# Optimization experiments

Hardware: AMD Instinct MI355X
Metric: run time of the kernel (lower is better)

The kernel has to match this reference:

```python
import jax, jax.numpy as jnp
import numpy as np

N_NODES = 50000
N_EDGES = 800000
DIM_FEAT = 96
INFO_DIM = 32
DIM_EMB = 160
CONV_OUT = DIM_EMB - INFO_DIM  # 128
NUM_LAYERS = 3
NUM_GRAPHS = 500
DIM_TARGET = 10


def setup_inputs() -> dict:
    key = jax.random.key(0)
    ks = jax.random.split(key, 20)
    inp = {
        'x': jax.random.normal(ks[0], (N_NODES, DIM_FEAT), dtype=jnp.float32),
        'edge_index': jax.random.randint(ks[1], (2, N_EDGES), 0, N_NODES, dtype=jnp.int32),
        'batch': jnp.sort(jax.random.randint(ks[2], (N_NODES,), 0, NUM_GRAPHS, dtype=jnp.int32)),
        'struc_info': jax.random.normal(ks[3], (NUM_GRAPHS, INFO_DIM), dtype=jnp.float32),
    }
    # SAGEConv params per layer: lin_l (on aggregated neighbors, with bias), lin_r (on root, no bias)
    in_dims = [DIM_FEAT + INFO_DIM, DIM_EMB, DIM_EMB]
    k = 4
    for i, din in enumerate(in_dims):
        s = 1.0 / np.sqrt(din)
        inp[f'Wl{i}'] = jax.random.uniform(ks[k], (din, CONV_OUT), jnp.float32, -s, s); k += 1
        inp[f'Wr{i}'] = jax.random.uniform(ks[k], (din, CONV_OUT), jnp.float32, -s, s); k += 1
        inp[f'b{i}'] = jax.random.uniform(ks[k], (CONV_OUT,), jnp.float32, -s, s); k += 1
    s1 = 1.0 / np.sqrt(NUM_LAYERS * CONV_OUT)
    inp['Wfc1'] = jax.random.uniform(ks[k], (NUM_LAYERS * CONV_OUT, DIM_EMB), jnp.float32, -s1, s1); k += 1
    inp['bfc1'] = jax.random.uniform(ks[k], (DIM_EMB,), jnp.float32, -s1, s1); k += 1
    s2 = 1.0 / np.sqrt(DIM_EMB)
    inp['Wfc2'] = jax.random.uniform(ks[k], (DIM_EMB, DIM_TARGET), jnp.float32, -s2, s2); k += 1
    inp['bfc2'] = jax.random.uniform(ks[k], (DIM_TARGET,), jnp.float32, -s2, s2)
    return inp


def _sage_conv(h, src, dst, Wl, Wr, b, n_nodes):
    # PyG SAGEConv (mean aggr): out = lin_l(mean_{j in N(i)} x_j) + lin_r(x_i)
    agg = jax.ops.segment_sum(h[src], dst, num_segments=n_nodes)       # [N, D]
    deg = jax.ops.segment_sum(jnp.ones_like(dst, dtype=h.dtype), dst, num_segments=n_nodes)
    mean = agg / jnp.maximum(deg, 1.0)[:, None]
    return mean @ Wl + b + h @ Wr


def reference(x, edge_index, batch, struc_info, Wl0, Wr0, b0, Wl1, Wr1, b1, Wl2, Wr2, b2, Wfc1, bfc1, Wfc2, bfc2):
    n_nodes = x.shape[0]
    src, dst = edge_index[0], edge_index[1]
    info = struc_info[batch]                         # [N, info_dim] repeated per node
    params = [(Wl0, Wr0, b0), (Wl1, Wr1, b1), (Wl2, Wr2, b2)]
    h = x
    outs = []
    for (Wl, Wr, b) in params:
        h = _sage_conv(jnp.concatenate([h, info], axis=1), src, dst, Wl, Wr, b, n_nodes)
        outs.append(h)
    hcat = jnp.concatenate(outs, axis=1)             # [N, num_layers*conv_out]
    g = jax.ops.segment_max(hcat, batch, num_segments=struc_info.shape[0])  # global max pool
    z = jax.nn.relu(g @ Wfc1 + bfc1)
    return z @ Wfc2 + bfc2
```

## Files before the change

### kernel.cpp

```cpp
#include <hip/hip_runtime.h>
#include <hip/hip_bf16.h>
#include <float.h>

#define NN 50000
#define NE 800000
#define DF 96
#define DI 32
#define CO 128
#define NG 500
#define F1I 384
#define F1O 160
#define F2O 10
#define CAPLOG 7
#define NRANGE 196
#define EPB 3125
#define RCAPLOG 13
#define GGEMM 391

typedef unsigned int  u32;
typedef unsigned short u16;
typedef short bf16x8 __attribute__((ext_vector_type(8)));
typedef float f32x4  __attribute__((ext_vector_type(4)));

__device__ __forceinline__ u16 f2b(float f) {
    __hip_bfloat16 h = __float2bfloat16(f);
    return *reinterpret_cast<u16*>(&h);
}
__device__ __forceinline__ float blo(u32 u) { return __uint_as_float(u << 16); }
__device__ __forceinline__ float bhi(u32 u) { return __uint_as_float(u & 0xffff0000u); }

struct P {
    const float* x; const int* batch; const float* info;
    const int* src; const int* dst;
    const float *Wl0, *Wr0, *b0, *Wl1, *Wr1, *b1, *Wl2, *Wr2, *b2;
    const float *Wfc1, *bfc1, *Wfc2, *bfc2;
    float* out;
    int* grescnt; u32* ebin; int* start; u16* xb;
    u16 *WT0, *WT1, *WT2;
    float *iQl0, *iQr0, *iQl1, *iQr1, *iQl2, *iQr2;
    int* cnt; u16* csr;
    u16 *h1, *h2, *h3, *zlp, *zq;
    float* gpart;
};


__device__ void sec_binA(int vb, const int* __restrict__ src, const int* __restrict__ dst,
                         int* __restrict__ grescnt, u32* __restrict__ ebin, char* smem) {
    u32* pairs = (u32*)smem;
    int* lcnt  = (int*)(smem + EPB * 4);
    int t = threadIdx.x;
    int base = vb * EPB;
    lcnt[t] = 0;
    __syncthreads();
    for (int j = t; j < EPB; j += 256) {
        int e = base + j;
        int d = dst[e];
        int s = src[e];
        pairs[j] = ((u32)(d & 255) << 24) | ((u32)(d >> 8) << 16) | (u32)s;
        atomicAdd(&lcnt[d >> 8], 1);
    }
    __syncthreads();
    int myCnt = lcnt[t];
    int myBase = atomicAdd(&grescnt[t * 16], myCnt);
    __syncthreads();
    lcnt[t] = myBase;
    __syncthreads();
    for (int j = t; j < EPB; j += 256) {
        u32 pr = pairs[j];
        int r = (pr >> 16) & 255;
        int pos = atomicAdd(&lcnt[r], 1);
        if (pos < (1 << RCAPLOG)) ebin[(r << RCAPLOG) + pos] = pr;
    }
}

__device__ void sec_starts(int vb, const int* __restrict__ batch, int* __restrict__ start) {
    int i = vb * 256 + threadIdx.x;
    if (i >= NN) return;
    int b = batch[i];
    if (i == 0) { for (int g = 0; g <= b; ++g) start[g] = 0; }
    else {
        int p = batch[i - 1];
        if (p != b) for (int g = p + 1; g <= b; ++g) start[g] = i;
    }
    if (i == NN - 1) { for (int g = b + 1; g <= NG; ++g) start[g] = NN; }
}

__device__ void sec_binB(int r, const u32* __restrict__ ebin, const int* __restrict__ grescnt,
                         int* __restrict__ cnt, u16* __restrict__ csr, char* smem) {
    int* lcnt = (int*)smem;
    int t = threadIdx.x;
    lcnt[t] = 0;
    __syncthreads();
    int total = grescnt[r * 16];
    if (total > (1 << RCAPLOG)) total = 1 << RCAPLOG;
    for (int j = t; j < total; j += 256) {
        u32 p = ebin[(r << RCAPLOG) + j];
        int dloc = p >> 24;
        int rank = atomicAdd(&lcnt[dloc], 1);
        int node = (r << 8) + dloc;
        if (rank < (1 << CAPLOG)) csr[(node << CAPLOG) + rank] = (u16)(p & 0xffff);
    }
    __syncthreads();
    int node = (r << 8) + t;
    if (node < NN) cnt[node] = lcnt[t];
}

__device__ void sec_cast(int vb, const float* __restrict__ x, u16* __restrict__ xb) {
    int tid = vb * 256 + threadIdx.x;
    if (tid >= NN * DF / 4) return;
    float4 v = *(const float4*)&x[tid * 4];
    ushort4 o;
    o.x = f2b(v.x); o.y = f2b(v.y); o.z = f2b(v.z); o.w = f2b(v.w);
    *(ushort4*)&xb[tid * 4] = o;
}

__device__ void sec_wt(int rel, const float* __restrict__ Wl, const float* __restrict__ Wr,
                       u16* __restrict__ WT, int K) {
    int tid = rel * 256 + threadIdx.x;
    if (tid >= 256 * K) return;
    int n = tid / K;
    int k = tid - n * K;
    float v = (n < CO) ? Wl[k * CO + n] : Wr[k * CO + (n - CO)];
    WT[tid] = f2b(v);
}

__device__ void sec_infow(int g, const float* __restrict__ info,
                          const float* __restrict__ Wl, const float* __restrict__ Wr,
                          const float* __restrict__ bias, int Ktop,
                          float* __restrict__ iQl, float* __restrict__ iQr) {
    int t = threadIdx.x;
    int c = t & 127;
    int sel = t >> 7;
    const float* W = sel ? Wr : Wl;
    float a = sel ? bias[c] : 0.0f;
    for (int d = 0; d < DI; ++d)
        a += info[g * DI + d] * W[(Ktop + d) * CO + c];
    (sel ? iQr : iQl)[g * CO + c] = a;
}

template<int K>
__device__ void sec_mfma(int vb, const u16* __restrict__ A, const u16* __restrict__ WTg,
                         const int* __restrict__ batch,
                         const float* __restrict__ iQl, const float* __restrict__ iQr,
                         u16* __restrict__ zlp, u16* __restrict__ zq, char* smem) {
    constexpr int PITCH = K + 8;
    short* lds = (short*)smem;

    int tid  = threadIdx.x;
    int w    = tid >> 6;
    int lane = tid & 63;
    int quad = lane >> 4;
    int l15  = lane & 15;

    constexpr int CH = 256 * K / 8;
    const uint4* wp = (const uint4*)WTg;
    for (int c = tid; c < CH; c += 256) {
        int n  = c / (K / 8);
        int ko = (c - n * (K / 8)) * 8;
        *(uint4*)&lds[n * PITCH + ko] = wp[c];
    }
    __syncthreads();

    int i0 = vb * 128 + w * 32;
    int r0 = i0 + l15;       if (r0 >= NN) r0 = NN - 1;
    int r1 = i0 + 16 + l15;  if (r1 >= NN) r1 = NN - 1;
    const short* A0 = (const short*)A + (size_t)r0 * K;
    const short* A1 = (const short*)A + (size_t)r1 * K;

    f32x4 acc[2][16];
#pragma unroll
    for (int rt = 0; rt < 2; ++rt)
#pragma unroll
        for (int ct = 0; ct < 16; ++ct)
            acc[rt][ct] = (f32x4){0.f, 0.f, 0.f, 0.f};

#pragma unroll
    for (int ks = 0; ks < K / 32; ++ks) {
        int ka = ks * 32 + quad * 8;
        bf16x8 a0 = *(const bf16x8*)(A0 + ka);
        bf16x8 a1 = *(const bf16x8*)(A1 + ka);
#pragma unroll
        for (int ct = 0; ct < 16; ++ct) {
            bf16x8 b = *(const bf16x8*)&lds[(ct * 16 + l15) * PITCH + ka];
            acc[0][ct] = __builtin_amdgcn_mfma_f32_16x16x32_bf16(a0, b, acc[0][ct], 0, 0, 0);
            acc[1][ct] = __builtin_amdgcn_mfma_f32_16x16x32_bf16(a1, b, acc[1][ct], 0, 0, 0);
        }
    }

#pragma unroll
    for (int rt = 0; rt < 2; ++rt) {
#pragma unroll
        for (int reg = 0; reg < 4; ++reg) {
            int row = i0 + rt * 16 + quad * 4 + reg;
            if (row < NN) {
                int b = batch[row];
                const float* ql = &iQl[b * CO];
                const float* qr = &iQr[b * CO];
                u16* lp = zlp + (size_t)row * CO;
                u16* qp = zq  + (size_t)row * CO;
#pragma unroll
                for (int ct = 0; ct < 8; ++ct) {
                    int col = ct * 16 + l15;
                    lp[col] = f2b(acc[rt][ct][reg] + ql[col]);
                }
#pragma unroll
                for (int ct = 8; ct < 16; ++ct) {
                    int col = ct * 16 + l15 - 128;
                    qp[col] = f2b(acc[rt][ct][reg] + qr[col]);
                }
            }
        }
    }
}

__device__ void sec_poolpart(int gr, const u32* __restrict__ hb, const int* __restrict__ start,
                             float* __restrict__ gpart, int off) {
    __shared__ float s_part[4][128];
    int t = threadIdx.x, w = t >> 6, lane = t & 63;
    int s = start[gr], e = start[gr + 1];
    float mlo = -FLT_MAX, mhi = -FLT_MAX;
    for (int n = s + w; n < e; n += 4) {
        u32 v = hb[(size_t)n * 64 + lane];
        mlo = fmaxf(mlo, blo(v)); mhi = fmaxf(mhi, bhi(v));
    }
    s_part[w][2 * lane]     = mlo;
    s_part[w][2 * lane + 1] = mhi;
    __syncthreads();
    if (t < 128) {
        float m = fmaxf(fmaxf(s_part[0][t], s_part[1][t]), fmaxf(s_part[2][t], s_part[3][t]));
        gpart[gr * 256 + off + t] = m;
    }
}

__device__ __forceinline__ void acc8(float* a, const uint4& u) {
    a[0] += blo(u.x); a[1] += bhi(u.x);
    a[2] += blo(u.y); a[3] += bhi(u.y);
    a[4] += blo(u.z); a[5] += bhi(u.z);
    a[6] += blo(u.w); a[7] += bhi(u.w);
}

__device__ void sec_gather(int vb, const u32* __restrict__ zlp, const u32* __restrict__ zq,
                           const int* __restrict__ cnt, const u16* __restrict__ csr,
                           u32* __restrict__ hout) {
    int wave = threadIdx.x >> 6;
    int lane = threadIdx.x & 63;
    int q    = lane >> 4;
    int l16  = lane & 15;
    int i = vb * 4 + wave;
    if (i >= NN) return;
    int deg = cnt[i];
    int degc = min(deg, 1 << CAPLOG);
    int s0 = i << CAPLOG;
    int s1 = s0 + degc;

    const uint4* Z = (const uint4*)zlp;

    float a[8] = {0,0,0,0,0,0,0,0};
    float b[8] = {0,0,0,0,0,0,0,0};
    float c[8] = {0,0,0,0,0,0,0,0};
    float d[8] = {0,0,0,0,0,0,0,0};

    int e = s0;
    for (; e + 15 < s1; e += 16) {
        int n0 = csr[e + q];
        int n1 = csr[e + 4 + q];
        int n2 = csr[e + 8 + q];
        int n3 = csr[e + 12 + q];
        uint4 u0 = Z[(size_t)n0 * 16 + l16];
        uint4 u1 = Z[(size_t)n1 * 16 + l16];
        uint4 u2 = Z[(size_t)n2 * 16 + l16];
        uint4 u3 = Z[(size_t)n3 * 16 + l16];
        acc8(a, u0); acc8(b, u1); acc8(c, u2); acc8(d, u3);
    }
    for (; e < s1; e += 4) {
        if (e + q < s1) {
            int n0 = csr[e + q];
            uint4 u0 = Z[(size_t)n0 * 16 + l16];
            acc8(a, u0);
        }
    }
#pragma unroll
    for (int j = 0; j < 8; ++j) {
        a[j] += b[j] + c[j] + d[j];
        a[j] += __shfl_xor(a[j], 16);
        a[j] += __shfl_xor(a[j], 32);
    }
    if (q == 0) {
        float r = 1.0f / fmaxf((float)deg, 1.0f);
        uint4 qq = ((const uint4*)zq)[(size_t)i * 16 + l16];
        uint4 o;
        o.x = (u32)f2b(a[0] * r + blo(qq.x)) | ((u32)f2b(a[1] * r + bhi(qq.x)) << 16);
        o.y = (u32)f2b(a[2] * r + blo(qq.y)) | ((u32)f2b(a[3] * r + bhi(qq.y)) << 16);
        o.z = (u32)f2b(a[4] * r + blo(qq.z)) | ((u32)f2b(a[5] * r + bhi(qq.z)) << 16);
        o.w = (u32)f2b(a[6] * r + blo(qq.w)) | ((u32)f2b(a[7] * r + bhi(qq.w)) << 16);
        ((uint4*)hout)[(size_t)i * 16 + l16] = o;
    }
}


#define PB_BIN    256
#define PB_STARTS 196
#define PB_CAST   4688
#define PB_WT     352
#define PB_INFO   1500
#define PREP_GRID (PB_BIN + PB_STARTS + PB_CAST + PB_WT + PB_INFO)

__global__ __launch_bounds__(256) void k_prep(P p) {
    __shared__ __align__(16) char smem[EPB * 4 + 1024];
    int blk = blockIdx.x;
    if (blk < PB_BIN) { sec_binA(blk, p.src, p.dst, p.grescnt, p.ebin, smem); return; }
    blk -= PB_BIN;
    if (blk < PB_STARTS) { sec_starts(blk, p.batch, p.start); return; }
    blk -= PB_STARTS;
    if (blk < PB_CAST) { sec_cast(blk, p.x, p.xb); return; }
    blk -= PB_CAST;
    if (blk < PB_WT) {
        if (blk < 96)       sec_wt(blk, p.Wl0, p.Wr0, p.WT0, 96);
        else if (blk < 224) sec_wt(blk - 96, p.Wl1, p.Wr1, p.WT1, 128);
        else                sec_wt(blk - 224, p.Wl2, p.Wr2, p.WT2, 128);
        return;
    }
    blk -= PB_WT;
    if (blk < 500)       sec_infow(blk, p.info, p.Wl0, p.Wr0, p.b0, 96,  p.iQl0, p.iQr0);
    else if (blk < 1000) sec_infow(blk - 500, p.info, p.Wl1, p.Wr1, p.b1, 128, p.iQl1, p.iQr1);
    else                 sec_infow(blk - 1000, p.info, p.Wl2, p.Wr2, p.b2, 128, p.iQl2, p.iQr2);
}

__global__ __launch_bounds__(256) void k_l0(P p) {
    __shared__ __align__(16) char smem[256 * (96 + 8) * 2];
    int blk = blockIdx.x;
    if (blk < NRANGE) sec_binB(blk, p.ebin, p.grescnt, p.cnt, p.csr, smem);
    else              sec_mfma<96>(blk - NRANGE, p.xb, p.WT0, p.batch, p.iQl0, p.iQr0,
                                   p.zlp, p.zq, smem);
}

__global__ __launch_bounds__(256) void k_l1(P p) {
    __shared__ __align__(16) char smem[256 * (128 + 8) * 2];
    int blk = blockIdx.x;
    if (blk < GGEMM) sec_mfma<128>(blk, p.h1, p.WT1, p.batch, p.iQl1, p.iQr1, p.zlp, p.zq, smem);
    else             sec_poolpart(blk - GGEMM, (const u32*)p.h1, p.start, p.gpart, 0);
}

__global__ __launch_bounds__(256) void k_l2(P p) {
    __shared__ __align__(16) char smem[256 * (128 + 8) * 2];
    int blk = blockIdx.x;
    if (blk < GGEMM) sec_mfma<128>(blk, p.h2, p.WT2, p.batch, p.iQl2, p.iQr2, p.zlp, p.zq, smem);
    else             sec_poolpart(blk - GGEMM, (const u32*)p.h2, p.start, p.gpart, 128);
}

__global__ __launch_bounds__(256) void k_g(P p, const u16* hout) {
    sec_gather(blockIdx.x, (const u32*)p.zlp, (const u32*)p.zq, p.cnt, p.csr, (u32*)hout);
}

__global__ __launch_bounds__(256) void k_pf(P p) {
    __shared__ float s_g[F1I];
    __shared__ float s_z[F1O];
    __shared__ float s_part[4][128];
    int gr = blockIdx.x;
    int t = threadIdx.x, w = t >> 6, lane = t & 63;
    int s = p.start[gr], e = p.start[gr + 1];
    const u32* hb = (const u32*)p.h3;
    float mlo = -FLT_MAX, mhi = -FLT_MAX;
    for (int n = s + w; n < e; n += 4) {
        u32 v = hb[(size_t)n * 64 + lane];
        mlo = fmaxf(mlo, blo(v)); mhi = fmaxf(mhi, bhi(v));
    }
    s_part[w][2 * lane]     = mlo;
    s_part[w][2 * lane + 1] = mhi;
    s_g[t] = p.gpart[gr * 256 + t];
    __syncthreads();
    if (t < 128)
        s_g[256 + t] = fmaxf(fmaxf(s_part[0][t], s_part[1][t]),
                             fmaxf(s_part[2][t], s_part[3][t]));
    __syncthreads();
    if (t < F1O) {
        float acc = p.bfc1[t];
        for (int k = 0; k < F1I; ++k) acc += s_g[k] * p.Wfc1[k * F1O + t];
        s_z[t] = fmaxf(acc, 0.0f);
    }
    __syncthreads();
    if (t < F2O) {
        float a = p.bfc2[t];
        for (int k = 0; k < F1O; ++k) a += s_z[k] * p.Wfc2[k * F2O + t];
        p.out[gr * F2O + t] = a;
    }
}

extern "C" void kernel_launch(void* const* d_in, const int* in_sizes, int n_in,
                              void* d_out, int out_size, void* d_ws, size_t ws_size,
                              hipStream_t stream) {
    const int* eidx = (const int*)d_in[1];

    char* W = (char*)d_ws;
    P p;
    p.x     = (const float*)d_in[0];
    p.batch = (const int*)d_in[2];
    p.info  = (const float*)d_in[3];
    p.src   = eidx;
    p.dst   = eidx + NE;
    p.Wl0 = (const float*)d_in[4];  p.Wr0 = (const float*)d_in[5];  p.b0 = (const float*)d_in[6];
    p.Wl1 = (const float*)d_in[7];  p.Wr1 = (const float*)d_in[8];  p.b1 = (const float*)d_in[9];
    p.Wl2 = (const float*)d_in[10]; p.Wr2 = (const float*)d_in[11]; p.b2 = (const float*)d_in[12];
    p.Wfc1 = (const float*)d_in[13]; p.bfc1 = (const float*)d_in[14];
    p.Wfc2 = (const float*)d_in[15]; p.bfc2 = (const float*)d_in[16];
    p.out = (float*)d_out;

    p.xb     = (u16*)(W + 0);
    p.h1     = (u16*)(W + 9600000);
    p.h2     = (u16*)(W + 22400000);
    p.h3     = (u16*)(W + 35200000);
    p.zlp    = (u16*)(W + 48000000);
    p.zq     = (u16*)(W + 60800000);
    p.WT0    = (u16*)(W + 73600000);
    p.WT1    = (u16*)(W + 73649152);
    p.WT2    = (u16*)(W + 73714688);
    p.iQl0   = (float*)(W + 73780224);
    p.iQr0   = (float*)(W + 74036224);
    p.iQl1   = (float*)(W + 74292224);
    p.iQr1   = (float*)(W + 74548224);
    p.iQl2   = (float*)(W + 74804224);
    p.iQr2   = (float*)(W + 75060224);
    p.start  = (int*)(W + 75316224);
    p.cnt    = (int*)(W + 75318272);
    p.csr    = (u16*)(W + 75518336);
    p.ebin   = (u32*)(W + 88318336);
    p.grescnt= (int*)(W + 96706560);
    p.gpart  = (float*)(W + 96722944);

    hipMemsetAsync(p.grescnt, 0, 256 * 16 * sizeof(int), stream);
    k_prep<<<PREP_GRID, 256, 0, stream>>>(p);
    k_l0<<<NRANGE + GGEMM, 256, 0, stream>>>(p);
    k_g<<<(NN + 3) / 4, 256, 0, stream>>>(p, p.h1);
    k_l1<<<GGEMM + NG, 256, 0, stream>>>(p);
    k_g<<<(NN + 3) / 4, 256, 0, stream>>>(p, p.h2);
    k_l2<<<GGEMM + NG, 256, 0, stream>>>(p);
    k_g<<<(NN + 3) / 4, 256, 0, stream>>>(p, p.h3);
    k_pf<<<NG, 256, 0, stream>>>(p);
}
```

Measured before the change: 357.2 us.

## Split binning out of layer-0 GEMM and fuse pooling into gather kernels

```diff
diff --git a/kernel.cpp b/kernel.cpp
--- a/kernel.cpp
+++ b/kernel.cpp
@@ -16,6 +16,7 @@
 #define EPB 3125
 #define RCAPLOG 13
 #define GGEMM 391
+#define GGATH 12500
 
 typedef unsigned int  u32;
 typedef unsigned short u16;
@@ -85,26 +86,6 @@
     if (i == NN - 1) { for (int g = b + 1; g <= NG; ++g) start[g] = NN; }
 }
 
-__device__ void sec_binB(int r, const u32* __restrict__ ebin, const int* __restrict__ grescnt,
-                         int* __restrict__ cnt, u16* __restrict__ csr, char* smem) {
-    int* lcnt = (int*)smem;
-    int t = threadIdx.x;
-    lcnt[t] = 0;
-    __syncthreads();
-    int total = grescnt[r * 16];
-    if (total > (1 << RCAPLOG)) total = 1 << RCAPLOG;
-    for (int j = t; j < total; j += 256) {
-        u32 p = ebin[(r << RCAPLOG) + j];
-        int dloc = p >> 24;
-        int rank = atomicAdd(&lcnt[dloc], 1);
-        int node = (r << 8) + dloc;
-        if (rank < (1 << CAPLOG)) csr[(node << CAPLOG) + rank] = (u16)(p & 0xffff);
-    }
-    __syncthreads();
-    int node = (r << 8) + t;
-    if (node < NN) cnt[node] = lcnt[t];
-}
-
 __device__ void sec_cast(int vb, const float* __restrict__ x, u16* __restrict__ xb) {
     int tid = vb * 256 + threadIdx.x;
     if (tid >= NN * DF / 4) return;
@@ -136,165 +117,6 @@
     for (int d = 0; d < DI; ++d)
         a += info[g * DI + d] * W[(Ktop + d) * CO + c];
     (sel ? iQr : iQl)[g * CO + c] = a;
-}
-
-template<int K>
-__device__ void sec_mfma(int vb, const u16* __restrict__ A, const u16* __restrict__ WTg,
-                         const int* __restrict__ batch,
-                         const float* __restrict__ iQl, const float* __restrict__ iQr,
-                         u16* __restrict__ zlp, u16* __restrict__ zq, char* smem) {
-    constexpr int PITCH = K + 8;
-    short* lds = (short*)smem;
-
-    int tid  = threadIdx.x;
-    int w    = tid >> 6;
-    int lane = tid & 63;
-    int quad = lane >> 4;
-    int l15  = lane & 15;
-
-    constexpr int CH = 256 * K / 8;
-    const uint4* wp = (const uint4*)WTg;
-    for (int c = tid; c < CH; c += 256) {
-        int n  = c / (K / 8);
-        int ko = (c - n * (K / 8)) * 8;
-        *(uint4*)&lds[n * PITCH + ko] = wp[c];
-    }
-    __syncthreads();
-
-    int i0 = vb * 128 + w * 32;
-    int r0 = i0 + l15;       if (r0 >= NN) r0 = NN - 1;
-    int r1 = i0 + 16 + l15;  if (r1 >= NN) r1 = NN - 1;
-    const short* A0 = (const short*)A + (size_t)r0 * K;
-    const short* A1 = (const short*)A + (size_t)r1 * K;
-
-    f32x4 acc[2][16];
-#pragma unroll
-    for (int rt = 0; rt < 2; ++rt)
-#pragma unroll
-        for (int ct = 0; ct < 16; ++ct)
-            acc[rt][ct] = (f32x4){0.f, 0.f, 0.f, 0.f};
-
-#pragma unroll
-    for (int ks = 0; ks < K / 32; ++ks) {
-        int ka = ks * 32 + quad * 8;
-        bf16x8 a0 = *(const bf16x8*)(A0 + ka);
-        bf16x8 a1 = *(const bf16x8*)(A1 + ka);
-#pragma unroll
-        for (int ct = 0; ct < 16; ++ct) {
-            bf16x8 b = *(const bf16x8*)&lds[(ct * 16 + l15) * PITCH + ka];
-            acc[0][ct] = __builtin_amdgcn_mfma_f32_16x16x32_bf16(a0, b, acc[0][ct], 0, 0, 0);
-            acc[1][ct] = __builtin_amdgcn_mfma_f32_16x16x32_bf16(a1, b, acc[1][ct], 0, 0, 0);
-        }
-    }
-
-#pragma unroll
-    for (int rt = 0; rt < 2; ++rt) {
-#pragma unroll
-        for (int reg = 0; reg < 4; ++reg) {
-            int row = i0 + rt * 16 + quad * 4 + reg;
-            if (row < NN) {
-                int b = batch[row];
-                const float* ql = &iQl[b * CO];
-                const float* qr = &iQr[b * CO];
-                u16* lp = zlp + (size_t)row * CO;
-                u16* qp = zq  + (size_t)row * CO;
-#pragma unroll
-                for (int ct = 0; ct < 8; ++ct) {
-                    int col = ct * 16 + l15;
-                    lp[col] = f2b(acc[rt][ct][reg] + ql[col]);
-                }
-#pragma unroll
-                for (int ct = 8; ct < 16; ++ct) {
-                    int col = ct * 16 + l15 - 128;
-                    qp[col] = f2b(acc[rt][ct][reg] + qr[col]);
-                }
-            }
-        }
-    }
-}
-
-__device__ void sec_poolpart(int gr, const u32* __restrict__ hb, const int* __restrict__ start,
-                             float* __restrict__ gpart, int off) {
-    __shared__ float s_part[4][128];
-    int t = threadIdx.x, w = t >> 6, lane = t & 63;
-    int s = start[gr], e = start[gr + 1];
-    float mlo = -FLT_MAX, mhi = -FLT_MAX;
-    for (int n = s + w; n < e; n += 4) {
-        u32 v = hb[(size_t)n * 64 + lane];
-        mlo = fmaxf(mlo, blo(v)); mhi = fmaxf(mhi, bhi(v));
-    }
-    s_part[w][2 * lane]     = mlo;
-    s_part[w][2 * lane + 1] = mhi;
-    __syncthreads();
-    if (t < 128) {
-        float m = fmaxf(fmaxf(s_part[0][t], s_part[1][t]), fmaxf(s_part[2][t], s_part[3][t]));
-        gpart[gr * 256 + off + t] = m;
-    }
-}
-
-__device__ __forceinline__ void acc8(float* a, const uint4& u) {
-    a[0] += blo(u.x); a[1] += bhi(u.x);
-    a[2] += blo(u.y); a[3] += bhi(u.y);
-    a[4] += blo(u.z); a[5] += bhi(u.z);
-    a[6] += blo(u.w); a[7] += bhi(u.w);
-}
-
-__device__ void sec_gather(int vb, const u32* __restrict__ zlp, const u32* __restrict__ zq,
-                           const int* __restrict__ cnt, const u16* __restrict__ csr,
-                           u32* __restrict__ hout) {
-    int wave = threadIdx.x >> 6;
-    int lane = threadIdx.x & 63;
-    int q    = lane >> 4;
-    int l16  = lane & 15;
-    int i = vb * 4 + wave;
-    if (i >= NN) return;
-    int deg = cnt[i];
-    int degc = min(deg, 1 << CAPLOG);
-    int s0 = i << CAPLOG;
-    int s1 = s0 + degc;
-
-    const uint4* Z = (const uint4*)zlp;
-
-    float a[8] = {0,0,0,0,0,0,0,0};
-    float b[8] = {0,0,0,0,0,0,0,0};
-    float c[8] = {0,0,0,0,0,0,0,0};
-    float d[8] = {0,0,0,0,0,0,0,0};
-
-    int e = s0;
-    for (; e + 15 < s1; e += 16) {
-        int n0 = csr[e + q];
-        int n1 = csr[e + 4 + q];
-        int n2 = csr[e + 8 + q];
-        int n3 = csr[e + 12 + q];
-        uint4 u0 = Z[(size_t)n0 * 16 + l16];
-        uint4 u1 = Z[(size_t)n1 * 16 + l16];
-        uint4 u2 = Z[(size_t)n2 * 16 + l16];
-        uint4 u3 = Z[(size_t)n3 * 16 + l16];
-        acc8(a, u0); acc8(b, u1); acc8(c, u2); acc8(d, u3);
-    }
-    for (; e < s1; e += 4) {
-        if (e + q < s1) {
-            int n0 = csr[e + q];
-            uint4 u0 = Z[(size_t)n0 * 16 + l16];
-            acc8(a, u0);
-        }
-    }
-#pragma unroll
-    for (int j = 0; j < 8; ++j) {
-        a[j] += b[j] + c[j] + d[j];
-        a[j] += __shfl_xor(a[j], 16);
-        a[j] += __shfl_xor(a[j], 32);
-    }
-    if (q == 0) {
-        float r = 1.0f / fmaxf((float)deg, 1.0f);
-        uint4 qq = ((const uint4*)zq)[(size_t)i * 16 + l16];
-        uint4 o;
-        o.x = (u32)f2b(a[0] * r + blo(qq.x)) | ((u32)f2b(a[1] * r + bhi(qq.x)) << 16);
-        o.y = (u32)f2b(a[2] * r + blo(qq.y)) | ((u32)f2b(a[3] * r + bhi(qq.y)) << 16);
-        o.z = (u32)f2b(a[4] * r + blo(qq.z)) | ((u32)f2b(a[5] * r + bhi(qq.z)) << 16);
-        o.w = (u32)f2b(a[6] * r + blo(qq.w)) | ((u32)f2b(a[7] * r + bhi(qq.w)) << 16);
-        ((uint4*)hout)[(size_t)i * 16 + l16] = o;
-    }
 }
 
 
@@ -326,30 +148,193 @@
     else                 sec_infow(blk - 1000, p.info, p.Wl2, p.Wr2, p.b2, 128, p.iQl2, p.iQr2);
 }
 
-__global__ __launch_bounds__(256) void k_l0(P p) {
-    __shared__ __align__(16) char smem[256 * (96 + 8) * 2];
-    int blk = blockIdx.x;
-    if (blk < NRANGE) sec_binB(blk, p.ebin, p.grescnt, p.cnt, p.csr, smem);
-    else              sec_mfma<96>(blk - NRANGE, p.xb, p.WT0, p.batch, p.iQl0, p.iQr0,
-                                   p.zlp, p.zq, smem);
-}
-
-__global__ __launch_bounds__(256) void k_l1(P p) {
-    __shared__ __align__(16) char smem[256 * (128 + 8) * 2];
-    int blk = blockIdx.x;
-    if (blk < GGEMM) sec_mfma<128>(blk, p.h1, p.WT1, p.batch, p.iQl1, p.iQr1, p.zlp, p.zq, smem);
-    else             sec_poolpart(blk - GGEMM, (const u32*)p.h1, p.start, p.gpart, 0);
-}
-
-__global__ __launch_bounds__(256) void k_l2(P p) {
-    __shared__ __align__(16) char smem[256 * (128 + 8) * 2];
-    int blk = blockIdx.x;
-    if (blk < GGEMM) sec_mfma<128>(blk, p.h2, p.WT2, p.batch, p.iQl2, p.iQr2, p.zlp, p.zq, smem);
-    else             sec_poolpart(blk - GGEMM, (const u32*)p.h2, p.start, p.gpart, 128);
+__global__ __launch_bounds__(256) void k_binB(P p) {
+    __shared__ int lcnt[256];
+    int r = blockIdx.x;
+    int t = threadIdx.x;
+    lcnt[t] = 0;
+    __syncthreads();
+    int total = p.grescnt[r * 16];
+    if (total > (1 << RCAPLOG)) total = 1 << RCAPLOG;
+    for (int j = t; j < total; j += 256) {
+        u32 pr = p.ebin[(r << RCAPLOG) + j];
+        int dloc = pr >> 24;
+        int rank = atomicAdd(&lcnt[dloc], 1);
+        int node = (r << 8) + dloc;
+        if (rank < (1 << CAPLOG)) p.csr[(node << CAPLOG) + rank] = (u16)(pr & 0xffff);
+    }
+    __syncthreads();
+    int node = (r << 8) + t;
+    if (node < NN) p.cnt[node] = lcnt[t];
+}
+
+template<int K>
+__global__ __launch_bounds__(256) void k_mfma(P p, const u16* __restrict__ A,
+                                              const u16* __restrict__ WTg,
+                                              const float* __restrict__ iQl,
+                                              const float* __restrict__ iQr) {
+    constexpr int PITCH = K + 8;
+    __shared__ short lds[256 * PITCH];
+
+    int tid  = threadIdx.x;
+    int w    = tid >> 6;
+    int lane = tid & 63;
+    int quad = lane >> 4;
+    int l15  = lane & 15;
+
+    constexpr int CH = 256 * K / 8;
+    const uint4* wp = (const uint4*)WTg;
+    for (int c = tid; c < CH; c += 256) {
+        int n  = c / (K / 8);
+        int ko = (c - n * (K / 8)) * 8;
+        *(uint4*)&lds[n * PITCH + ko] = wp[c];
+    }
+    __syncthreads();
+
+    int i0 = blockIdx.x * 128 + w * 32;
+    int r0 = i0 + l15;       if (r0 >= NN) r0 = NN - 1;
+    int r1 = i0 + 16 + l15;  if (r1 >= NN) r1 = NN - 1;
+    const short* A0 = (const short*)A + (size_t)r0 * K;
+    const short* A1 = (const short*)A + (size_t)r1 * K;
+
+    f32x4 acc[2][16];
+#pragma unroll
+    for (int rt = 0; rt < 2; ++rt)
+#pragma unroll
+        for (int ct = 0; ct < 16; ++ct)
+            acc[rt][ct] = (f32x4){0.f, 0.f, 0.f, 0.f};
+
+#pragma unroll
+    for (int ks = 0; ks < K / 32; ++ks) {
+        int ka = ks * 32 + quad * 8;
+        bf16x8 a0 = *(const bf16x8*)(A0 + ka);
+        bf16x8 a1 = *(const bf16x8*)(A1 + ka);
+#pragma unroll
+        for (int ct = 0; ct < 16; ++ct) {
+            bf16x8 b = *(const bf16x8*)&lds[(ct * 16 + l15) * PITCH + ka];
+            acc[0][ct] = __builtin_amdgcn_mfma_f32_16x16x32_bf16(a0, b, acc[0][ct], 0, 0, 0);
+            acc[1][ct] = __builtin_amdgcn_mfma_f32_16x16x32_bf16(a1, b, acc[1][ct], 0, 0, 0);
+        }
+    }
+
+#pragma unroll
+    for (int rt = 0; rt < 2; ++rt) {
+#pragma unroll
+        for (int reg = 0; reg < 4; ++reg) {
+            int row = i0 + rt * 16 + quad * 4 + reg;
+            if (row < NN) {
+                int b = p.batch[row];
+                const float* ql = &iQl[b * CO];
+                const float* qr = &iQr[b * CO];
+                u16* lp = p.zlp + (size_t)row * CO;
+                u16* qp = p.zq  + (size_t)row * CO;
+#pragma unroll
+                for (int ct = 0; ct < 8; ++ct) {
+                    int col = ct * 16 + l15;
+                    lp[col] = f2b(acc[rt][ct][reg] + ql[col]);
+                }
+#pragma unroll
+                for (int ct = 8; ct < 16; ++ct) {
+                    int col = ct * 16 + l15 - 128;
+                    qp[col] = f2b(acc[rt][ct][reg] + qr[col]);
+                }
+            }
+        }
+    }
+}
+
+__device__ __forceinline__ void acc8(float* a, const uint4& u) {
+    a[0] += blo(u.x); a[1] += bhi(u.x);
+    a[2] += blo(u.y); a[3] += bhi(u.y);
+    a[4] += blo(u.z); a[5] += bhi(u.z);
+    a[6] += blo(u.w); a[7] += bhi(u.w);
+}
+
+__device__ void sec_gather(int vb, const u32* __restrict__ zlp, const u32* __restrict__ zq,
+                           const int* __restrict__ cnt, const u16* __restrict__ csr,
+                           u32* __restrict__ hout) {
+    int wave = threadIdx.x >> 6;
+    int lane = threadIdx.x & 63;
+    int q    = lane >> 4;
+    int l16  = lane & 15;
+    int i = vb * 4 + wave;
+    if (i >= NN) return;
+    int deg = cnt[i];
+    int degc = min(deg, 1 << CAPLOG);
+    int s0 = i << CAPLOG;
+    int s1 = s0 + degc;
+
+    const uint4* Z = (const uint4*)zlp;
+
+    float a[8] = {0,0,0,0,0,0,0,0};
+    float b[8] = {0,0,0,0,0,0,0,0};
+    float c[8] = {0,0,0,0,0,0,0,0};
+    float d[8] = {0,0,0,0,0,0,0,0};
+
+    int e = s0;
+    for (; e + 15 < s1; e += 16) {
+        int n0 = csr[e + q];
+        int n1 = csr[e + 4 + q];
+        int n2 = csr[e + 8 + q];
+        int n3 = csr[e + 12 + q];
+        uint4 u0 = Z[(size_t)n0 * 16 + l16];
+        uint4 u1 = Z[(size_t)n1 * 16 + l16];
+        uint4 u2 = Z[(size_t)n2 * 16 + l16];
+        uint4 u3 = Z[(size_t)n3 * 16 + l16];
+        acc8(a, u0); acc8(b, u1); acc8(c, u2); acc8(d, u3);
+    }
+    for (; e < s1; e += 4) {
+        if (e + q < s1) {
+            int n0 = csr[e + q];
+            uint4 u0 = Z[(size_t)n0 * 16 + l16];
+            acc8(a, u0);
+        }
+    }
+#pragma unroll
+    for (int j = 0; j < 8; ++j) {
+        a[j] += b[j] + c[j] + d[j];
+        a[j] += __shfl_xor(a[j], 16);
+        a[j] += __shfl_xor(a[j], 32);
+    }
+    if (q == 0) {
+        float r = 1.0f / fmaxf((float)deg, 1.0f);
+        uint4 qq = ((const uint4*)zq)[(size_t)i * 16 + l16];
+        uint4 o;
+        o.x = (u32)f2b(a[0] * r + blo(qq.x)) | ((u32)f2b(a[1] * r + bhi(qq.x)) << 16);
+        o.y = (u32)f2b(a[2] * r + blo(qq.y)) | ((u32)f2b(a[3] * r + bhi(qq.y)) << 16);
+        o.z = (u32)f2b(a[4] * r + blo(qq.z)) | ((u32)f2b(a[5] * r + bhi(qq.z)) << 16);
+        o.w = (u32)f2b(a[6] * r + blo(qq.w)) | ((u32)f2b(a[7] * r + bhi(qq.w)) << 16);
+        ((uint4*)hout)[(size_t)i * 16 + l16] = o;
+    }
+}
+
+__device__ void sec_poolpart(int gr, const u32* __restrict__ hb, const int* __restrict__ start,
+                             float* __restrict__ gpart, int off) {
+    __shared__ float s_part[4][128];
+    int t = threadIdx.x, w = t >> 6, lane = t & 63;
+    int s = start[gr], e = start[gr + 1];
+    float mlo = -FLT_MAX, mhi = -FLT_MAX;
+    for (int n = s + w; n < e; n += 4) {
+        u32 v = hb[(size_t)n * 64 + lane];
+        mlo = fmaxf(mlo, blo(v)); mhi = fmaxf(mhi, bhi(v));
+    }
+    s_part[w][2 * lane]     = mlo;
+    s_part[w][2 * lane + 1] = mhi;
+    __syncthreads();
+    if (t < 128) {
+        float m = fmaxf(fmaxf(s_part[0][t], s_part[1][t]), fmaxf(s_part[2][t], s_part[3][t]));
+        gpart[gr * 256 + off + t] = m;
+    }
 }
 
 __global__ __launch_bounds__(256) void k_g(P p, const u16* hout) {
     sec_gather(blockIdx.x, (const u32*)p.zlp, (const u32*)p.zq, p.cnt, p.csr, (u32*)hout);
+}
+
+__global__ __launch_bounds__(256) void k_gp(P p, const u16* hout, const u16* hpool, int off) {
+    int blk = blockIdx.x;
+    if (blk < GGATH) sec_gather(blk, (const u32*)p.zlp, (const u32*)p.zq, p.cnt, p.csr, (u32*)hout);
+    else             sec_poolpart(blk - GGATH, (const u32*)hpool, p.start, p.gpart, off);
 }
 
 __global__ __launch_bounds__(256) void k_pf(P p) {
@@ -429,11 +414,16 @@
 
     hipMemsetAsync(p.grescnt, 0, 256 * 16 * sizeof(int), stream);
     k_prep<<<PREP_GRID, 256, 0, stream>>>(p);
-    k_l0<<<NRANGE + GGEMM, 256, 0, stream>>>(p);
-    k_g<<<(NN + 3) / 4, 256, 0, stream>>>(p, p.h1);
-    k_l1<<<GGEMM + NG, 256, 0, stream>>>(p);
-    k_g<<<(NN + 3) / 4, 256, 0, stream>>>(p, p.h2);
-    k_l2<<<GGEMM + NG, 256, 0, stream>>>(p);
-    k_g<<<(NN + 3) / 4, 256, 0, stream>>>(p, p.h3);
+    k_binB<<<NRANGE, 256, 0, stream>>>(p);
+
+    k_mfma<96><<<GGEMM, 256, 0, stream>>>(p, p.xb, p.WT0, p.iQl0, p.iQr0);
+    k_g<<<GGATH, 256, 0, stream>>>(p, p.h1);
+
+    k_mfma<128><<<GGEMM, 256, 0, stream>>>(p, p.h1, p.WT1, p.iQl1, p.iQr1);
+    k_gp<<<GGATH + NG, 256, 0, stream>>>(p, p.h2, p.h1, 0);
+
+    k_mfma<128><<<GGEMM, 256, 0, stream>>>(p, p.h2, p.WT2, p.iQl2, p.iQr2);
+    k_gp<<<GGATH + NG, 256, 0, stream>>>(p, p.h3, p.h2, 128);
+
     k_pf<<<NG, 256, 0, stream>>>(p);
 }
```

New measurement: 313.3 us. 1.14x faster.

## Move per-layer max pooling into final pool+FC kernel and drop pooling blocks

Applied to the files above, without the earlier changes.

```diff
diff --git a/kernel.cpp b/kernel.cpp
--- a/kernel.cpp
+++ b/kernel.cpp
@@ -16,6 +16,7 @@
 #define EPB 3125
 #define RCAPLOG 13
 #define GGEMM 391
+#define GGATH 12500
 
 typedef unsigned int  u32;
 typedef unsigned short u16;
@@ -40,7 +41,6 @@
     float *iQl0, *iQr0, *iQl1, *iQr1, *iQl2, *iQr2;
     int* cnt; u16* csr;
     u16 *h1, *h2, *h3, *zlp, *zq;
-    float* gpart;
 };
 
 
@@ -213,88 +213,11 @@
     }
 }
 
-__device__ void sec_poolpart(int gr, const u32* __restrict__ hb, const int* __restrict__ start,
-                             float* __restrict__ gpart, int off) {
-    __shared__ float s_part[4][128];
-    int t = threadIdx.x, w = t >> 6, lane = t & 63;
-    int s = start[gr], e = start[gr + 1];
-    float mlo = -FLT_MAX, mhi = -FLT_MAX;
-    for (int n = s + w; n < e; n += 4) {
-        u32 v = hb[(size_t)n * 64 + lane];
-        mlo = fmaxf(mlo, blo(v)); mhi = fmaxf(mhi, bhi(v));
-    }
-    s_part[w][2 * lane]     = mlo;
-    s_part[w][2 * lane + 1] = mhi;
-    __syncthreads();
-    if (t < 128) {
-        float m = fmaxf(fmaxf(s_part[0][t], s_part[1][t]), fmaxf(s_part[2][t], s_part[3][t]));
-        gpart[gr * 256 + off + t] = m;
-    }
-}
-
 __device__ __forceinline__ void acc8(float* a, const uint4& u) {
     a[0] += blo(u.x); a[1] += bhi(u.x);
     a[2] += blo(u.y); a[3] += bhi(u.y);
     a[4] += blo(u.z); a[5] += bhi(u.z);
     a[6] += blo(u.w); a[7] += bhi(u.w);
-}
-
-__device__ void sec_gather(int vb, const u32* __restrict__ zlp, const u32* __restrict__ zq,
-                           const int* __restrict__ cnt, const u16* __restrict__ csr,
-                           u32* __restrict__ hout) {
-    int wave = threadIdx.x >> 6;
-    int lane = threadIdx.x & 63;
-    int q    = lane >> 4;
-    int l16  = lane & 15;
-    int i = vb * 4 + wave;
-    if (i >= NN) return;
-    int deg = cnt[i];
-    int degc = min(deg, 1 << CAPLOG);
-    int s0 = i << CAPLOG;
-    int s1 = s0 + degc;
-
-    const uint4* Z = (const uint4*)zlp;
-
-    float a[8] = {0,0,0,0,0,0,0,0};
-    float b[8] = {0,0,0,0,0,0,0,0};
-    float c[8] = {0,0,0,0,0,0,0,0};
-    float d[8] = {0,0,0,0,0,0,0,0};
-
-    int e = s0;
-    for (; e + 15 < s1; e += 16) {
-        int n0 = csr[e + q];
-        int n1 = csr[e + 4 + q];
-        int n2 = csr[e + 8 + q];
-        int n3 = csr[e + 12 + q];
-        uint4 u0 = Z[(size_t)n0 * 16 + l16];
-        uint4 u1 = Z[(size_t)n1 * 16 + l16];
-        uint4 u2 = Z[(size_t)n2 * 16 + l16];
-        uint4 u3 = Z[(size_t)n3 * 16 + l16];
-        acc8(a, u0); acc8(b, u1); acc8(c, u2); acc8(d, u3);
-    }
-    for (; e < s1; e += 4) {
-        if (e + q < s1) {
-            int n0 = csr[e + q];
-            uint4 u0 = Z[(size_t)n0 * 16 + l16];
-            acc8(a, u0);
-        }
-    }
-#pragma unroll
-    for (int j = 0; j < 8; ++j) {
-        a[j] += b[j] + c[j] + d[j];
-        a[j] += __shfl_xor(a[j], 16);
-        a[j] += __shfl_xor(a[j], 32);
-    }
-    if (q == 0) {
-        float r = 1.0f / fmaxf((float)deg, 1.0f);
-        uint4 qq = ((const uint4*)zq)[(size_t)i * 16 + l16];
-        uint4 o;
-        o.x = (u32)f2b(a[0] * r + blo(qq.x)) | ((u32)f2b(a[1] * r + bhi(qq.x)) << 16);
-        o.y = (u32)f2b(a[2] * r + blo(qq.y)) | ((u32)f2b(a[3] * r + bhi(qq.y)) << 16);
-        o.z = (u32)f2b(a[4] * r + blo(qq.z)) | ((u32)f2b(a[5] * r + bhi(qq.z)) << 16);
-        o.w = (u32)f2b(a[6] * r + blo(qq.w)) | ((u32)f2b(a[7] * r + bhi(qq.w)) << 16);
-        ((uint4*)hout)[(size_t)i * 16 + l16] = o;
-    }
 }
 
 
@@ -334,44 +257,114 @@
                                    p.zlp, p.zq, smem);
 }
 
-__global__ __launch_bounds__(256) void k_l1(P p) {
+__global__ __launch_bounds__(256) void k_mfma128(P p, const u16* __restrict__ A,
+                                                 const u16* __restrict__ WTg,
+                                                 const float* __restrict__ iQl,
+                                                 const float* __restrict__ iQr) {
     __shared__ __align__(16) char smem[256 * (128 + 8) * 2];
-    int blk = blockIdx.x;
-    if (blk < GGEMM) sec_mfma<128>(blk, p.h1, p.WT1, p.batch, p.iQl1, p.iQr1, p.zlp, p.zq, smem);
-    else             sec_poolpart(blk - GGEMM, (const u32*)p.h1, p.start, p.gpart, 0);
-}
-
-__global__ __launch_bounds__(256) void k_l2(P p) {
-    __shared__ __align__(16) char smem[256 * (128 + 8) * 2];
-    int blk = blockIdx.x;
-    if (blk < GGEMM) sec_mfma<128>(blk, p.h2, p.WT2, p.batch, p.iQl2, p.iQr2, p.zlp, p.zq, smem);
-    else             sec_poolpart(blk - GGEMM, (const u32*)p.h2, p.start, p.gpart, 128);
-}
-
-__global__ __launch_bounds__(256) void k_g(P p, const u16* hout) {
-    sec_gather(blockIdx.x, (const u32*)p.zlp, (const u32*)p.zq, p.cnt, p.csr, (u32*)hout);
-}
-
-__global__ __launch_bounds__(256) void k_pf(P p) {
+    sec_mfma<128>(blockIdx.x, A, WTg, p.batch, iQl, iQr, p.zlp, p.zq, smem);
+}
+
+__global__ __launch_bounds__(256) void k_g(P p, u16* hout) {
+    int wave = threadIdx.x >> 6;
+    int lane = threadIdx.x & 63;
+    int q    = lane >> 4;
+    int l16  = lane & 15;
+    int i = blockIdx.x * 4 + wave;
+    if (i >= NN) return;
+    int deg = p.cnt[i];
+    int degc = min(deg, 1 << CAPLOG);
+    int s0 = i << CAPLOG;
+    int s1 = s0 + degc;
+
+    const uint4* Z = (const uint4*)p.zlp;
+    const u16* csr = p.csr;
+
+    float a[8] = {0,0,0,0,0,0,0,0};
+    float b[8] = {0,0,0,0,0,0,0,0};
+    float c[8] = {0,0,0,0,0,0,0,0};
+    float d[8] = {0,0,0,0,0,0,0,0};
+
+    int e = s0;
+    for (; e + 15 < s1; e += 16) {
+        int n0 = csr[e + q];
+        int n1 = csr[e + 4 + q];
+        int n2 = csr[e + 8 + q];
+        int n3 = csr[e + 12 + q];
+        uint4 u0 = Z[(size_t)n0 * 16 + l16];
+        uint4 u1 = Z[(size_t)n1 * 16 + l16];
+        uint4 u2 = Z[(size_t)n2 * 16 + l16];
+        uint4 u3 = Z[(size_t)n3 * 16 + l16];
+        acc8(a, u0); acc8(b, u1); acc8(c, u2); acc8(d, u3);
+    }
+    for (; e < s1; e += 4) {
+        if (e + q < s1) {
+            int n0 = csr[e + q];
+            uint4 u0 = Z[(size_t)n0 * 16 + l16];
+            acc8(a, u0);
+        }
+    }
+#pragma unroll
+    for (int j = 0; j < 8; ++j) {
+        a[j] += b[j] + c[j] + d[j];
+        a[j] += __shfl_xor(a[j], 16);
+        a[j] += __shfl_xor(a[j], 32);
+    }
+    if (q == 0) {
+        float r = 1.0f / fmaxf((float)deg, 1.0f);
+        uint4 qq = ((const uint4*)p.zq)[(size_t)i * 16 + l16];
+        uint4 o;
+        o.x = (u32)f2b(a[0] * r + blo(qq.x)) | ((u32)f2b(a[1] * r + bhi(qq.x)) << 16);
+        o.y = (u32)f2b(a[2] * r + blo(qq.y)) | ((u32)f2b(a[3] * r + bhi(qq.y)) << 16);
+        o.z = (u32)f2b(a[4] * r + blo(qq.z)) | ((u32)f2b(a[5] * r + bhi(qq.z)) << 16);
+        o.w = (u32)f2b(a[6] * r + blo(qq.w)) | ((u32)f2b(a[7] * r + bhi(qq.w)) << 16);
+        ((uint4*)hout)[(size_t)i * 16 + l16] = o;
+    }
+}
+
+__global__ __launch_bounds__(384) void k_poolfc(P p) {
+    __shared__ float s_part[6][128];
     __shared__ float s_g[F1I];
     __shared__ float s_z[F1O];
-    __shared__ float s_part[4][128];
     int gr = blockIdx.x;
-    int t = threadIdx.x, w = t >> 6, lane = t & 63;
+    int t  = threadIdx.x;
+    int w    = t >> 6;
+    int lane = t & 63;
+    int buf  = w % 3;
+    int half = w / 3;
+    const u32* hb = (buf == 0) ? (const u32*)p.h1 : (buf == 1) ? (const u32*)p.h2 : (const u32*)p.h3;
     int s = p.start[gr], e = p.start[gr + 1];
-    const u32* hb = (const u32*)p.h3;
-    float mlo = -FLT_MAX, mhi = -FLT_MAX;
-    for (int n = s + w; n < e; n += 4) {
-        u32 v = hb[(size_t)n * 64 + lane];
-        mlo = fmaxf(mlo, blo(v)); mhi = fmaxf(mhi, bhi(v));
-    }
-    s_part[w][2 * lane]     = mlo;
-    s_part[w][2 * lane + 1] = mhi;
-    s_g[t] = p.gpart[gr * 256 + t];
-    __syncthreads();
-    if (t < 128)
-        s_g[256 + t] = fmaxf(fmaxf(s_part[0][t], s_part[1][t]),
-                             fmaxf(s_part[2][t], s_part[3][t]));
+    int mid = (s + e) >> 1;
+    int n0 = half ? mid : s;
+    int n1 = half ? e : mid;
+
+    float mlo[4], mhi[4];
+#pragma unroll
+    for (int j = 0; j < 4; ++j) { mlo[j] = -FLT_MAX; mhi[j] = -FLT_MAX; }
+    int n = n0;
+    for (; n + 3 < n1; n += 4) {
+        u32 v0 = hb[(size_t)(n + 0) * 64 + lane];
+        u32 v1 = hb[(size_t)(n + 1) * 64 + lane];
+        u32 v2 = hb[(size_t)(n + 2) * 64 + lane];
+        u32 v3 = hb[(size_t)(n + 3) * 64 + lane];
+        mlo[0] = fmaxf(mlo[0], blo(v0)); mhi[0] = fmaxf(mhi[0], bhi(v0));
+        mlo[1] = fmaxf(mlo[1], blo(v1)); mhi[1] = fmaxf(mhi[1], bhi(v1));
+        mlo[2] = fmaxf(mlo[2], blo(v2)); mhi[2] = fmaxf(mhi[2], bhi(v2));
+        mlo[3] = fmaxf(mlo[3], blo(v3)); mhi[3] = fmaxf(mhi[3], bhi(v3));
+    }
+    for (; n < n1; ++n) {
+        u32 v0 = hb[(size_t)n * 64 + lane];
+        mlo[0] = fmaxf(mlo[0], blo(v0)); mhi[0] = fmaxf(mhi[0], bhi(v0));
+    }
+    float lo = fmaxf(fmaxf(mlo[0], mlo[1]), fmaxf(mlo[2], mlo[3]));
+    float hi = fmaxf(fmaxf(mhi[0], mhi[1]), fmaxf(mhi[2], mhi[3]));
+    s_part[w][2 * lane]     = lo;
+    s_part[w][2 * lane + 1] = hi;
+    __syncthreads();
+    {
+        int buf2 = t >> 7, cc = t & 127;
+        s_g[t] = fmaxf(s_part[buf2][cc], s_part[buf2 + 3][cc]);
+    }
     __syncthreads();
     if (t < F1O) {
         float acc = p.bfc1[t];
@@ -425,15 +418,18 @@
     p.csr    = (u16*)(W + 75518336);
     p.ebin   = (u32*)(W + 88318336);
     p.grescnt= (int*)(W + 96706560);
-    p.gpart  = (float*)(W + 96722944);
 
     hipMemsetAsync(p.grescnt, 0, 256 * 16 * sizeof(int), stream);
     k_prep<<<PREP_GRID, 256, 0, stream>>>(p);
+
     k_l0<<<NRANGE + GGEMM, 256, 0, stream>>>(p);
-    k_g<<<(NN + 3) / 4, 256, 0, stream>>>(p, p.h1);
-    k_l1<<<GGEMM + NG, 256, 0, stream>>>(p);
-    k_g<<<(NN + 3) / 4, 256, 0, stream>>>(p, p.h2);
-    k_l2<<<GGEMM + NG, 256, 0, stream>>>(p);
-    k_g<<<(NN + 3) / 4, 256, 0, stream>>>(p, p.h3);
-    k_pf<<<NG, 256, 0, stream>>>(p);
-}
+    k_g<<<GGATH, 256, 0, stream>>>(p, p.h1);
+
+    k_mfma128<<<GGEMM, 256, 0, stream>>>(p, p.h1, p.WT1, p.iQl1, p.iQr1);
+    k_g<<<GGATH, 256, 0, stream>>>(p, p.h2);
+
+    k_mfma128<<<GGEMM, 256, 0, stream>>>(p, p.h2, p.WT2, p.iQl2, p.iQr2);
+    k_g<<<GGATH, 256, 0, stream>>>(p, p.h3);
+
+    k_poolfc<<<NG, 384, 0, stream>>>(p);
+}
```

After: 301.7 us. -15.6%, faster.
